# Optimization experiments

Measured on AMD Instinct MI355X. Metric: run time of the kernel, lower is better.

## Reference

```python
import jax, jax.numpy as jnp
import numpy as np

IN_C = 256
OUT_C = 256
K_NUM = 6
EDGE_TYPE = 3


def setup_inputs() -> dict:
    key = jax.random.key(0)
    k1, k2, k3, k4, k5 = jax.random.split(key, 5)
    N, T, V = 32, 64, 25
    x = jax.random.normal(k1, (N, IN_C, T, V), dtype=jnp.float32)
    A = jax.random.uniform(k2, (K_NUM - EDGE_TYPE, V, V), dtype=jnp.float32)
    B = jax.random.uniform(k3, (N, EDGE_TYPE, V, V), dtype=jnp.float32)
    lamda_act = jnp.float32(0.5)
    # ConvTranspose2d with kernel (1,1), stride 1, no padding == pointwise matmul.
    # torch weight shape (in, out, 1, 1) -> store squeezed (in, out).
    W = jax.random.normal(k4, (IN_C, OUT_C * K_NUM), dtype=jnp.float32) * (1.0 / np.sqrt(IN_C))
    b = jax.random.normal(k5, (OUT_C * K_NUM,), dtype=jnp.float32) * 0.01
    return {"x": x, "A": A, "B": B, "lamda_act": lamda_act, "W": W, "b": b}


def reference(x, A, B, lamda_act, W, b):
    # pointwise transposed conv (1x1 kernel) -> channel matmul
    y = jnp.einsum('nctv,co->notv', x, W) + b[None, :, None, None]  # [N, K*C_out, T, V]
    n, kc, t, v = y.shape
    y = y.reshape(n, K_NUM, kc // K_NUM, t, v)
    x1 = jnp.einsum('nkctv,kvw->nctw', y[:, :K_NUM - EDGE_TYPE], A)
    x2 = jnp.einsum('nkctv,nkvw->nctw', y[:, K_NUM - EDGE_TYPE:], B)
    x_sum = x1 + x2 * lamda_act
    return (x_sum, A)
```

## Files before the change

kernel.cpp:

```cpp
#include <hip/hip_runtime.h>
#include <hip/hip_bf16.h>
#include <stdint.h>

typedef __bf16 bf16_t;
typedef bf16_t bf16x8 __attribute__((ext_vector_type(8)));
typedef float f32x4 __attribute__((ext_vector_type(4)));

#define DEVI static __device__ __forceinline__

constexpr int NB = 32, CIN = 256, COUT = 256, KNUM = 6, ET = 3, TDIM = 64, VV = 25;
constexpr int KD   = KNUM * CIN;
constexpr long OUT0 = (long)NB * COUT * TDIM * VV;
constexpr int ACNT = ET * VV * VV;

constexpr int NSTEP = 24;
constexpr int WP3_CHUNKS = NSTEP * 2048;
constexpr size_t WP3_BYTES  = (size_t)WP3_CHUNKS * 16;
constexpr size_t BIAS_OFF   = WP3_BYTES;
constexpr size_t BIAS_BYTES = (size_t)NB * VV * COUT * 4;
constexpr size_t WS_NEED    = BIAS_OFF + BIAS_BYTES;

DEVI unsigned packbf(float lo, float hi) {
  unsigned short a = __builtin_bit_cast(unsigned short, (bf16_t)lo);
  unsigned short b = __builtin_bit_cast(unsigned short, (bf16_t)hi);
  return ((unsigned)b << 16) | (unsigned)a;
}

__global__ __launch_bounds__(256) void prep_kernel(
    const float* __restrict__ A, const float* __restrict__ Bm,
    const float* __restrict__ lam_p, const float* __restrict__ W,
    const float* __restrict__ bvec, bf16_t* __restrict__ wp3,
    float* __restrict__ biasmat, float* __restrict__ outA)
{
  int idx = blockIdx.x * 256 + threadIdx.x;
  constexpr int S1 = WP3_CHUNKS;
  constexpr int S2 = S1 + NB * VV * COUT;
  constexpr int S3 = S2 + ACNT;
  if (idx < S1) {
    int s  = idx >> 11;
    int r  = idx & 2047;
    int mi = r >> 7;
    int kk = (r >> 6) & 1;
    int ln = r & 63;
    int lg = ln >> 4, lw = ln & 15;
    int cb = s / 6, k = s - cb * 6;
    int cibase = cb * 64 + (lg + 4 * kk) * 8;
    int col = (k << 8) + mi * 16 + lw;
    bf16_t* dst = wp3 + ((long)idx << 3);
    #pragma unroll
    for (int e = 0; e < 8; ++e)
      dst[e] = (bf16_t)W[(cibase + e) * KD + col];
  } else if (idx < S2) {
    int j = idx - S1;
    int c = j & 255;
    int nw = j >> 8;
    int w = nw % VV;
    int n = nw / VV;
    float lam = lam_p[0];
    float s = 0.f;
    for (int k = 0; k < KNUM; ++k) {
      float sk = 0.f;
      if (k < ET) {
        for (int v = 0; v < VV; ++v) sk += A[(k * VV + v) * VV + w];
      } else {
        for (int v = 0; v < VV; ++v) sk += Bm[(((n * ET) + (k - ET)) * VV + v) * VV + w];
        sk *= lam;
      }
      s += bvec[(k << 8) + c] * sk;
    }
    biasmat[j] = s;
  } else if (idx < S3) {
    int j = idx - S2;
    outA[j] = A[j];
  }
}

__global__ __launch_bounds__(512, 2) void fused_kernel(
    const float* __restrict__ x, const float* __restrict__ A,
    const float* __restrict__ Bm, const float* __restrict__ lam_p,
    const bf16_t* __restrict__ wp3, const float* __restrict__ biasmat,
    float* __restrict__ out)
{
  __shared__ bf16_t Bs[2 * 128 * 64];
  __shared__ bf16_t Xs[256 * 32];
  __shared__ bf16_t Ms[KNUM * 32 * 32];

  const int b = blockIdx.x;
  const int n = b >> 4;
  const int t0 = (b & 15) << 2;
  const int tid = threadIdx.x;
  const int wv = tid >> 6, ln = tid & 63;
  const int lw = ln & 15, lg = ln >> 4;
  const float lam = lam_p[0];

  for (int i = tid; i < KNUM * 32 * 32; i += 512) {
    int R = i >> 5, v = i & 31;
    int k = i >> 10, w = (i >> 5) & 31;
    float val = 0.f;
    if (w < VV && v < VV)
      val = (k < ET) ? A[(k * VV + v) * VV + w]
                     : lam * Bm[(((n * ET) + (k - ET)) * VV + v) * VV + w];
    int sw2 = (w & 3) ^ ((w >> 2) & 3);
    int byteoff = R * 64 + ((((v >> 3) ^ sw2) & 3) << 4) + ((v & 7) << 1);
    *(bf16_t*)((char*)Ms + byteoff) = (bf16_t)val;
  }

  f32x4 acc[4][4] = {};
  const int m_base = (wv >> 1) * 64;
  const int mb4 = (wv >> 1) * 4;
  const int n_base = (wv & 1) * 64;
  const f32x4 z4 = {0.f, 0.f, 0.f, 0.f};
  const int msw2 = (lw & 3) ^ ((lw >> 2) & 3);

  for (int cb = 0; cb < 4; ++cb) {
    if (tid < 256) {
      int ci = tid >> 2, dt = tid & 3;
      const float* xp = x + ((long)(n * CIN + cb * 64 + ci) * TDIM + t0 + dt) * VV;
      float xv[25];
      #pragma unroll
      for (int v = 0; v < VV; ++v) xv[v] = xp[v];
      int row = dt * 64 + ci;
      int sw = (row & 3) ^ ((row >> 2) & 3);
      #pragma unroll
      for (int g = 0; g < 4; ++g) {
        char* base = (char*)Xs + row * 64 + ((g ^ sw) & 3) * 16;
        #pragma unroll
        for (int p = 0; p < 4; ++p) {
          int v0 = g * 8 + p * 2;
          float lo = (v0     < VV) ? xv[v0 < VV ? v0 : 0]     : 0.f;
          float hi = (v0 + 1 < VV) ? xv[v0 + 1 < VV ? v0 + 1 : 0] : 0.f;
          *(unsigned*)(base + p * 4) = packbf(lo, hi);
        }
      }
    }
    __syncthreads();

    for (int k = 0; k < KNUM; ++k) {
      const int s = cb * 6 + k;
      const int buf = (s & 1) * (128 * 64);
      bf16x8 af2[2][4];
      const bf16_t* wpS = wp3 + (((long)s * 2048 + (long)mb4 * 128 + ln) << 3);
      #pragma unroll
      for (int kk = 0; kk < 2; ++kk)
        #pragma unroll
        for (int i = 0; i < 4; ++i)
          af2[kk][i] = *(const bf16x8*)(wpS + ((i * 128 + kk * 64) << 3));

      bf16x8 mb0 = *(const bf16x8*)((const char*)Ms + (k * 32 + lw) * 64 + (((lg ^ msw2) & 3) << 4));
      bf16x8 mb1 = *(const bf16x8*)((const char*)Ms + (k * 32 + 16 + lw) * 64 + (((lg ^ msw2) & 3) << 4));
      #pragma unroll
      for (int rt = 0; rt < 2; ++rt) {
        int arow = wv * 32 + rt * 16 + lw;
        int sw = (arow & 3) ^ ((arow >> 2) & 3);
        bf16x8 af = *(const bf16x8*)((const char*)Xs + arow * 64 + ((lg ^ sw) & 3) * 16);
        f32x4 d0 = __builtin_amdgcn_mfma_f32_16x16x32_bf16(af, mb0, z4, 0, 0, 0);
        f32x4 d1 = __builtin_amdgcn_mfma_f32_16x16x32_bf16(af, mb1, z4, 0, 0, 0);
        int rbase = wv * 32 + rt * 16 + (lg << 2);
        int dt = rbase >> 6, ci0 = rbase & 63;
        int r0 = dt * 32 + lw;
        int g0 = ((ci0 >> 3) ^ (r0 & 7)) & 7;
        char* c0 = (char*)(Bs + buf) + r0 * 128 + (g0 << 4) + ((ci0 << 1) & 15);
        *(unsigned*)(c0)     = packbf(d0[0], d0[1]);
        *(unsigned*)(c0 + 4) = packbf(d0[2], d0[3]);
        int r1 = r0 + 16;
        char* c1 = (char*)(Bs + buf) + r1 * 128 + (g0 << 4) + ((ci0 << 1) & 15);
        *(unsigned*)(c1)     = packbf(d1[0], d1[1]);
        *(unsigned*)(c1 + 4) = packbf(d1[2], d1[3]);
      }
      __syncthreads();

      __builtin_amdgcn_s_setprio(1);
      #pragma unroll
      for (int kk = 0; kk < 2; ++kk) {
        bf16x8 bf2[4];
        #pragma unroll
        for (int j = 0; j < 4; ++j) {
          int rr = n_base + j * 16 + lw;
          int gg = ((kk * 4 + lg) ^ (rr & 7)) & 7;
          bf2[j] = *(const bf16x8*)((const char*)(Bs + buf) + rr * 128 + (gg << 4));
        }
        #pragma unroll
        for (int i = 0; i < 4; ++i)
          #pragma unroll
          for (int j = 0; j < 4; ++j)
            acc[i][j] = __builtin_amdgcn_mfma_f32_16x16x32_bf16(af2[kk][i], bf2[j], acc[i][j], 0, 0, 0);
      }
      __builtin_amdgcn_s_setprio(0);
    }
  }

  #pragma unroll
  for (int j = 0; j < 4; ++j) {
    int colb = n_base + j * 16 + lw;
    int dt = colb >> 5, w = colb & 31;
    if (w < VV) {
      float* ob = out + (long)n * 409600 + (t0 + dt) * 25 + w;
      const float* brow = biasmat + (n * 25 + w) * 256;
      #pragma unroll
      for (int i = 0; i < 4; ++i) {
        int mb = m_base + i * 16 + (lg << 2);
        #pragma unroll
        for (int r = 0; r < 4; ++r) {
          int m = mb + r;
          ob[(long)m * 1600] = acc[i][j][r] + brow[m];
        }
      }
    }
  }
}

__global__ __launch_bounds__(256) void fallback_kernel(
    const float* __restrict__ x, const float* __restrict__ A,
    const float* __restrict__ Bm, const float* __restrict__ lam_p,
    const float* __restrict__ W, const float* __restrict__ bvec,
    float* __restrict__ out)
{
  __shared__ __align__(16) float xs[CIN][28];
  __shared__ __align__(16) float Ms[KNUM][VV][28];
  const int nt = blockIdx.x;
  const int n = nt >> 6, t = nt & 63;
  const int tid = threadIdx.x;
  const float lam = lam_p[0];

  const float* xp = x + (((long)(n * CIN + tid) * TDIM + t) * VV);
  #pragma unroll
  for (int v = 0; v < VV; ++v) xs[tid][v] = xp[v];
  xs[tid][25] = xs[tid][26] = xs[tid][27] = 0.f;
  for (int i = tid; i < KNUM * VV * VV; i += 256) {
    int k = i / (VV * VV);
    int r = i - k * VV * VV;
    int v = r / VV;
    int w = r - v * VV;
    Ms[k][v][w] = (k < ET) ? A[(k * VV + v) * VV + w]
                           : lam * Bm[(((n * ET) + (k - ET)) * VV + v) * VV + w];
    if (w == 24) { Ms[k][v][25] = Ms[k][v][26] = Ms[k][v][27] = 0.f; }
  }
  __syncthreads();

  float oacc[28] = {};
  for (int k = 0; k < KNUM; ++k) {
    float yv[28];
    float bv = bvec[(k << 8) + tid];
    #pragma unroll
    for (int v = 0; v < 28; ++v) yv[v] = 0.f;
    for (int ci = 0; ci < CIN; ++ci) {
      float wl = W[ci * KD + (k << 8) + tid];
      const f32x4* x4 = (const f32x4*)&xs[ci][0];
      #pragma unroll
      for (int q = 0; q < 7; ++q) {
        f32x4 xv = x4[q];
        yv[q*4+0] += wl*xv[0]; yv[q*4+1] += wl*xv[1];
        yv[q*4+2] += wl*xv[2]; yv[q*4+3] += wl*xv[3];
      }
    }
    #pragma unroll
    for (int v = 0; v < VV; ++v) {
      float yvv = yv[v] + bv;
      const f32x4* m4 = (const f32x4*)&Ms[k][v][0];
      #pragma unroll
      for (int q = 0; q < 7; ++q) {
        f32x4 mv = m4[q];
        oacc[q*4+0] += yvv*mv[0]; oacc[q*4+1] += yvv*mv[1];
        oacc[q*4+2] += yvv*mv[2]; oacc[q*4+3] += yvv*mv[3];
      }
    }
  }
  float* op = out + (((long)(n * COUT + tid) * TDIM + t) * VV);
  #pragma unroll
  for (int w = 0; w < VV; ++w) op[w] = oacc[w];
}

__global__ void copyA_kernel(const float* __restrict__ A, float* __restrict__ outA) {
  int i = blockIdx.x * 256 + threadIdx.x;
  if (i < ACNT) outA[i] = A[i];
}

extern "C" void kernel_launch(void* const* d_in, const int* in_sizes, int n_in,
                              void* d_out, int out_size, void* d_ws, size_t ws_size,
                              hipStream_t stream) {
  const float* x   = (const float*)d_in[0];
  const float* A   = (const float*)d_in[1];
  const float* Bm  = (const float*)d_in[2];
  const float* lam = (const float*)d_in[3];
  const float* W   = (const float*)d_in[4];
  const float* bv  = (const float*)d_in[5];
  float* out = (float*)d_out;

  if (d_ws != nullptr && ws_size >= WS_NEED) {
    bf16_t* wp3     = (bf16_t*)d_ws;
    float*  biasmat = (float*)((char*)d_ws + BIAS_OFF);
    constexpr int PREP_ITEMS = WP3_CHUNKS + NB * VV * COUT + ACNT;
    prep_kernel<<<(PREP_ITEMS + 255) / 256, 256, 0, stream>>>(A, Bm, lam, W, bv, wp3, biasmat, out + OUT0);
    fused_kernel<<<NB * 16, 512, 0, stream>>>(x, A, Bm, lam, wp3, biasmat, out);
  } else {
    fallback_kernel<<<NB * TDIM, 256, 0, stream>>>(x, A, Bm, lam, W, bv, out);
    copyA_kernel<<<(ACNT + 255) / 256, 256, 0, stream>>>(A, out + OUT0);
  }
}
```

Baseline: 84.55 us.

## Software-pipeline weight loads and first-stage MFMA with second-stage GEMM

```diff
diff --git a/kernel.cpp b/kernel.cpp
--- a/kernel.cpp
+++ b/kernel.cpp
@@ -81,9 +81,9 @@
     const bf16_t* __restrict__ wp3, const float* __restrict__ biasmat,
     float* __restrict__ out)
 {
-  __shared__ bf16_t Bs[2 * 128 * 64];
-  __shared__ bf16_t Xs[256 * 32];
-  __shared__ bf16_t Ms[KNUM * 32 * 32];
+  __shared__ __align__(16) bf16_t Bs[2 * 128 * 64];
+  __shared__ __align__(16) bf16_t Xs[256 * 32];
+  __shared__ __align__(16) bf16_t Ms[KNUM * 32 * 32];
 
   const int b = blockIdx.x;
   const int n = b >> 4;
@@ -112,7 +112,63 @@
   const f32x4 z4 = {0.f, 0.f, 0.f, 0.f};
   const int msw2 = (lw & 3) ^ ((lw >> 2) & 3);
 
+  auto compute1 = [&](int k, uint2* pk) {
+    bf16x8 mb0 = *(const bf16x8*)((const char*)Ms + (k * 32 + lw) * 64 + (((lg ^ msw2) & 3) << 4));
+    bf16x8 mb1 = *(const bf16x8*)((const char*)Ms + (k * 32 + 16 + lw) * 64 + (((lg ^ msw2) & 3) << 4));
+    #pragma unroll
+    for (int rt = 0; rt < 2; ++rt) {
+      int arow = wv * 32 + rt * 16 + lw;
+      int sw = (arow & 3) ^ ((arow >> 2) & 3);
+      int off = ((lg ^ sw) & 3) << 4;
+      bf16x8 af = *(const bf16x8*)((const char*)Xs + arow * 64 + off);
+      f32x4 d0 = __builtin_amdgcn_mfma_f32_16x16x32_bf16(af, mb0, z4, 0, 0, 0);
+      f32x4 d1 = __builtin_amdgcn_mfma_f32_16x16x32_bf16(af, mb1, z4, 0, 0, 0);
+      uint2 p0; p0.x = packbf(d0[0], d0[1]); p0.y = packbf(d0[2], d0[3]);
+      uint2 p1; p1.x = packbf(d1[0], d1[1]); p1.y = packbf(d1[2], d1[3]);
+      pk[rt * 2 + 0] = p0;
+      pk[rt * 2 + 1] = p1;
+    }
+  };
+  auto loadaf2 = [&](int s, bf16x8 af[2][4]) {
+    const bf16_t* wpS = wp3 + (((long)s * 2048 + (long)mb4 * 128 + ln) << 3);
+    #pragma unroll
+    for (int kk = 0; kk < 2; ++kk)
+      #pragma unroll
+      for (int i = 0; i < 4; ++i)
+        af[kk][i] = *(const bf16x8*)(wpS + ((i * 128 + kk * 64) << 3));
+  };
+  auto writepk = [&](int buf, const uint2* pk) {
+    #pragma unroll
+    for (int rt = 0; rt < 2; ++rt) {
+      int rbase = wv * 32 + rt * 16 + (lg << 2);
+      int dt = rbase >> 6, ci0 = rbase & 63;
+      int r0 = dt * 32 + lw;
+      int g0 = ((ci0 >> 3) ^ (r0 & 7)) & 7;
+      *(uint2*)((char*)(Bs + buf) + r0 * 128 + (g0 << 4) + ((ci0 << 1) & 15)) = pk[rt * 2 + 0];
+      *(uint2*)((char*)(Bs + buf) + (r0 + 16) * 128 + (g0 << 4) + ((ci0 << 1) & 15)) = pk[rt * 2 + 1];
+    }
+  };
+  auto mfma2 = [&](int buf, bf16x8 af[2][4]) {
+    #pragma unroll
+    for (int kk = 0; kk < 2; ++kk) {
+      bf16x8 bf2[4];
+      #pragma unroll
+      for (int j = 0; j < 4; ++j) {
+        int rr = n_base + j * 16 + lw;
+        int gg = ((kk * 4 + lg) ^ (rr & 7)) & 7;
+        bf2[j] = *(const bf16x8*)((const char*)(Bs + buf) + rr * 128 + (gg << 4));
+      }
+      #pragma unroll
+      for (int i = 0; i < 4; ++i)
+        #pragma unroll
+        for (int j = 0; j < 4; ++j)
+          acc[i][j] = __builtin_amdgcn_mfma_f32_16x16x32_bf16(af[kk][i], bf2[j], acc[i][j], 0, 0, 0);
+    }
+  };
+
+  #pragma unroll 1
   for (int cb = 0; cb < 4; ++cb) {
+    __syncthreads();
     if (tid < 256) {
       int ci = tid >> 2, dt = tid & 3;
       const float* xp = x + ((long)(n * CIN + cb * 64 + ci) * TDIM + t0 + dt) * VV;
@@ -135,57 +191,30 @@
     }
     __syncthreads();
 
+    uint2 pk[4];
+    bf16x8 af2[2][4];
+    compute1(0, pk);
+    loadaf2(cb * 6, af2);
+
+    #pragma unroll
     for (int k = 0; k < KNUM; ++k) {
       const int s = cb * 6 + k;
       const int buf = (s & 1) * (128 * 64);
-      bf16x8 af2[2][4];
-      const bf16_t* wpS = wp3 + (((long)s * 2048 + (long)mb4 * 128 + ln) << 3);
-      #pragma unroll
-      for (int kk = 0; kk < 2; ++kk)
+      writepk(buf, pk);
+      __syncthreads();
+      bf16x8 af2n[2][4];
+      if (k < KNUM - 1) loadaf2(s + 1, af2n);
+      __builtin_amdgcn_s_setprio(1);
+      mfma2(buf, af2);
+      if (k < KNUM - 1) compute1(k + 1, pk);
+      __builtin_amdgcn_s_setprio(0);
+      if (k < KNUM - 1) {
         #pragma unroll
-        for (int i = 0; i < 4; ++i)
-          af2[kk][i] = *(const bf16x8*)(wpS + ((i * 128 + kk * 64) << 3));
-
-      bf16x8 mb0 = *(const bf16x8*)((const char*)Ms + (k * 32 + lw) * 64 + (((lg ^ msw2) & 3) << 4));
-      bf16x8 mb1 = *(const bf16x8*)((const char*)Ms + (k * 32 + 16 + lw) * 64 + (((lg ^ msw2) & 3) << 4));
-      #pragma unroll
-      for (int rt = 0; rt < 2; ++rt) {
-        int arow = wv * 32 + rt * 16 + lw;
-        int sw = (arow & 3) ^ ((arow >> 2) & 3);
-        bf16x8 af = *(const bf16x8*)((const char*)Xs + arow * 64 + ((lg ^ sw) & 3) * 16);
-        f32x4 d0 = __builtin_amdgcn_mfma_f32_16x16x32_bf16(af, mb0, z4, 0, 0, 0);
-        f32x4 d1 = __builtin_amdgcn_mfma_f32_16x16x32_bf16(af, mb1, z4, 0, 0, 0);
-        int rbase = wv * 32 + rt * 16 + (lg << 2);
-        int dt = rbase >> 6, ci0 = rbase & 63;
-        int r0 = dt * 32 + lw;
-        int g0 = ((ci0 >> 3) ^ (r0 & 7)) & 7;
-        char* c0 = (char*)(Bs + buf) + r0 * 128 + (g0 << 4) + ((ci0 << 1) & 15);
-        *(unsigned*)(c0)     = packbf(d0[0], d0[1]);
-        *(unsigned*)(c0 + 4) = packbf(d0[2], d0[3]);
-        int r1 = r0 + 16;
-        char* c1 = (char*)(Bs + buf) + r1 * 128 + (g0 << 4) + ((ci0 << 1) & 15);
-        *(unsigned*)(c1)     = packbf(d1[0], d1[1]);
-        *(unsigned*)(c1 + 4) = packbf(d1[2], d1[3]);
-      }
-      __syncthreads();
-
-      __builtin_amdgcn_s_setprio(1);
-      #pragma unroll
-      for (int kk = 0; kk < 2; ++kk) {
-        bf16x8 bf2[4];
-        #pragma unroll
-        for (int j = 0; j < 4; ++j) {
-          int rr = n_base + j * 16 + lw;
-          int gg = ((kk * 4 + lg) ^ (rr & 7)) & 7;
-          bf2[j] = *(const bf16x8*)((const char*)(Bs + buf) + rr * 128 + (gg << 4));
-        }
-        #pragma unroll
-        for (int i = 0; i < 4; ++i)
+        for (int kk = 0; kk < 2; ++kk)
           #pragma unroll
-          for (int j = 0; j < 4; ++j)
-            acc[i][j] = __builtin_amdgcn_mfma_f32_16x16x32_bf16(af2[kk][i], bf2[j], acc[i][j], 0, 0, 0);
-      }
-      __builtin_amdgcn_s_setprio(0);
+          for (int i = 0; i < 4; ++i)
+            af2[kk][i] = af2n[kk][i];
+      }
     }
   }
 
```

Result: slower. 89.18 us (+5.5%).
